# Performance work log

Hardware: AMD Instinct MI355X
Metric: run time of the kernel (lower is better)

## Reference

```python
import jax, jax.numpy as jnp
import numpy as np

WS, SS, NH = 7, 3, 16  # window_size, shift_size, num_heads


def _rel_pos_index(ws):
    coords = np.stack(np.meshgrid(np.arange(ws), np.arange(ws), indexing='ij'))  # (2, ws, ws)
    cf = coords.reshape(2, -1)                       # (2, N)
    rel = (cf[:, :, None] - cf[:, None, :]).transpose(1, 2, 0).copy()  # (N, N, 2)
    rel[:, :, 0] += ws - 1
    rel[:, :, 1] += ws - 1
    rel[:, :, 0] *= 2 * ws - 1
    return rel.sum(-1)                               # (N, N) int indices into bias table


def _attn_mask(Hp, Wp, ws, ss):
    img = np.zeros((Hp, Wp))
    slices = (slice(0, -ws), slice(-ws, -ss), slice(-ss, None))
    cnt = 0
    for h in slices:
        for w in slices:
            img[h, w] = cnt
            cnt += 1
    mw = img.reshape(Hp // ws, ws, Wp // ws, ws).transpose(0, 2, 1, 3).reshape(-1, ws * ws)  # (nW, N)
    am = mw[:, None, :] - mw[:, :, None]             # (nW, N, N)
    return np.where(am != 0, -100.0, 0.0).astype(np.float32)


def setup_inputs() -> dict:
    key = jax.random.key(0)
    k1, k2, k3, k4 = jax.random.split(key, 4)
    B, H, W, C = 16, 56, 56, 512
    return {
        'q_out': jax.random.normal(k1, (B, H, W, C), dtype=jnp.float32),
        'k_out': jax.random.normal(k2, (B, H, W, C), dtype=jnp.float32),
        'v_out': jax.random.normal(k3, (B, H, W, C), dtype=jnp.float32),
        'bias_table': 0.02 * jax.random.normal(k4, ((2 * WS - 1) ** 2, NH), dtype=jnp.float32),
        'C': C, 'H': H, 'W': W,
        'x_low_padding_h': 0, 'x_low_padding_w': 0,
    }


def reference(q_out, k_out, v_out, bias_table, C, H, W, x_low_padding_h, x_low_padding_w):
    ws, ss, nh = WS, SS, NH
    Hp, Wp = H + x_low_padding_h, W + x_low_padding_w
    B = q_out.shape[0]
    hd = C // nh
    scale = hd ** (-0.5)
    N = ws * ws

    def part(x):  # (B,Hp,Wp,C) -> (B*nW, N, C)
        x = x.reshape(B, Hp // ws, ws, Wp // ws, ws, C).transpose(0, 1, 3, 2, 4, 5)
        return x.reshape(-1, N, C)

    # cyclic shift
    sq = jnp.roll(q_out, (-ss, -ss), axis=(1, 2))
    sk = jnp.roll(k_out, (-ss, -ss), axis=(1, 2))
    sv = jnp.roll(v_out, (-ss, -ss), axis=(1, 2))

    qw, kw, vw = part(sq), part(sk), part(sv)
    B_ = qw.shape[0]
    q = qw.reshape(B_, N, nh, hd).transpose(0, 2, 1, 3) * scale  # (B_, nh, N, hd)
    k = kw.reshape(B_, N, nh, hd).transpose(0, 2, 1, 3)
    v = vw.reshape(B_, N, nh, hd).transpose(0, 2, 1, 3)

    attn = jnp.einsum('bhnd,bhmd->bhnm', q, k)  # (B_, nh, N, N)

    # relative position bias
    rpi = _rel_pos_index(ws)
    bias = bias_table[rpi.reshape(-1)].reshape(N, N, nh).transpose(2, 0, 1)  # (nh, N, N)
    attn = attn + bias[None]

    # shift mask
    am = jnp.asarray(_attn_mask(Hp, Wp, ws, ss), dtype=attn.dtype)  # (nW, N, N)
    nW = am.shape[0]
    attn = attn.reshape(B_ // nW, nW, nh, N, N) + am[None, :, None]
    attn = jax.nn.softmax(attn.reshape(B_, nh, N, N), axis=-1)

    xw = jnp.einsum('bhnm,bhmd->bhnd', attn, v).transpose(0, 2, 1, 3).reshape(B_, N, C)

    # window reverse + reverse shift
    x = xw.reshape(B, Hp // ws, Wp // ws, ws, ws, C).transpose(0, 1, 3, 2, 4, 5).reshape(B, Hp, Wp, C)
    return jnp.roll(x, (ss, ss), axis=(1, 2))
```

## Files before the change

### kernel.cpp

```cpp
#include <hip/hip_runtime.h>
#include <stdint.h>


constexpr int WSZ  = 7;
constexpr int NTOK = 49;
constexpr int NH_  = 16;
constexpr int HD_  = 32;
constexpr int SP   = 56;
constexpr int CH   = 512;
constexpr float LOG2E = 1.4426950408889634f;

typedef float    f32x4 __attribute__((ext_vector_type(4)));
typedef short    s16x8 __attribute__((ext_vector_type(8)));
typedef _Float16 f16x4 __attribute__((ext_vector_type(4)));

union FragU { uint32_t w[4]; s16x8 v; };

__device__ __forceinline__ uint32_t bf16_hibits(float x) {
    uint32_t u = __float_as_uint(x);
    u += 0x7fffu + ((u >> 16) & 1u);
    return u & 0xffff0000u;
}
__device__ __forceinline__ uint32_t pk_bf16(float a, float b) {
    return (bf16_hibits(a) >> 16) | bf16_hibits(b);
}

__global__ __launch_bounds__(256)
void build_bm(const float* __restrict__ bias, _Float16* __restrict__ bm)
{
    const int blk = blockIdx.x;
    const int h = blk >> 2, cls = blk & 3;
    for (int idx = threadIdx.x; idx < 4096; idx += 256) {
        const int q = idx >> 6, m = idx & 63;
        float val;
        if (q >= NTOK || m >= NTOK) {
            val = -1000.0f;
        } else {
            const int iq = q / 7, jq = q % 7, im = m / 7, jm = m % 7;
            const int rpi = (iq - im + 6) * 13 + (jq - jm + 6);
            const float bv = bias[rpi * NH_ + h];
            const int rq = ((cls & 2) ? (iq < 4 ? 3 : 6) : 0)
                         + ((cls & 1) ? (jq < 4 ? 1 : 2) : 0);
            const int rm = ((cls & 2) ? (im < 4 ? 3 : 6) : 0)
                         + ((cls & 1) ? (jm < 4 ? 1 : 2) : 0);
            const float mask = (rq != rm) ? -100.0f : 0.0f;
            val = (bv + mask) * LOG2E;
        }
        bm[blk * 4096 + idx] = (_Float16)val;
    }
}

struct Raw {
    float4 q[4][2];
    float4 k[4][2];
    float  v[2][2][8];
};
struct Frag {
    s16x8 Qh[4], Kh[4], Vb[2][2];
};

__device__ __forceinline__ int make_off(int wh, int lane) {
    const int h  = wh & 15;
    const int w  = wh >> 4;
    const int wc = w & 7, wr = (w >> 3) & 7, b = w >> 6;
    const int t  = lane < NTOK ? lane : NTOK - 1;
    const int it = t / 7, jt = t - 7 * it;
    int sr = wr * 7 + it + 3; if (sr >= SP) sr -= SP;
    int sc = wc * 7 + jt + 3; if (sc >= SP) sc -= SP;
    return ((b * SP + sr) * SP + sc) * CH + h * HD_;
}
__device__ __forceinline__ int cls_of(int wh) {
    const int w = wh >> 4;
    return ((((w >> 3) & 7) == 7) ? 2 : 0) | (((w & 7) == 7) ? 1 : 0);
}

__device__ __forceinline__ void issue_qkv(const float* __restrict__ qg,
                                          const float* __restrict__ kg,
                                          const float* __restrict__ vg,
                                          int off, int l16, int g, Raw& r) {
    int oQK[4];
#pragma unroll
    for (int tt = 0; tt < 4; ++tt) oQK[tt] = __shfl(off, 16 * tt + l16);
    int oV[16];
#pragma unroll
    for (int mc = 0; mc < 2; ++mc)
#pragma unroll
        for (int e = 0; e < 8; ++e) oV[8 * mc + e] = __shfl(off, 32 * mc + 8 * g + e);
#pragma unroll
    for (int tt = 0; tt < 4; ++tt) {
        const float* qp = qg + oQK[tt] + 8 * g;
        const float* kp = kg + oQK[tt] + 8 * g;
        r.q[tt][0] = *(const float4*)qp;  r.q[tt][1] = *(const float4*)(qp + 4);
        r.k[tt][0] = *(const float4*)kp;  r.k[tt][1] = *(const float4*)(kp + 4);
    }
#pragma unroll
    for (int mc = 0; mc < 2; ++mc)
#pragma unroll
        for (int dh = 0; dh < 2; ++dh)
#pragma unroll
            for (int e = 0; e < 8; ++e)
                r.v[mc][dh][e] = vg[oV[8 * mc + e] + 16 * dh + l16];
}

__device__ __forceinline__ void convertQKV(const Raw& r, float qs, Frag& f) {
#pragma unroll
    for (int tt = 0; tt < 4; ++tt) {
        FragU qh, kh;
        qh.w[0] = pk_bf16(r.q[tt][0].x * qs, r.q[tt][0].y * qs);
        qh.w[1] = pk_bf16(r.q[tt][0].z * qs, r.q[tt][0].w * qs);
        qh.w[2] = pk_bf16(r.q[tt][1].x * qs, r.q[tt][1].y * qs);
        qh.w[3] = pk_bf16(r.q[tt][1].z * qs, r.q[tt][1].w * qs);
        kh.w[0] = pk_bf16(r.k[tt][0].x, r.k[tt][0].y);
        kh.w[1] = pk_bf16(r.k[tt][0].z, r.k[tt][0].w);
        kh.w[2] = pk_bf16(r.k[tt][1].x, r.k[tt][1].y);
        kh.w[3] = pk_bf16(r.k[tt][1].z, r.k[tt][1].w);
        f.Qh[tt] = qh.v; f.Kh[tt] = kh.v;
    }
#pragma unroll
    for (int mc = 0; mc < 2; ++mc)
#pragma unroll
        for (int dh = 0; dh < 2; ++dh) {
            FragU fu;
#pragma unroll
            for (int wd = 0; wd < 4; ++wd)
                fu.w[wd] = pk_bf16(r.v[mc][dh][2 * wd], r.v[mc][dh][2 * wd + 1]);
            f.Vb[mc][dh] = fu.v;
        }
}

__device__ __forceinline__ void load_bm(const _Float16* __restrict__ bmh,
                                        int l16, int g, f16x4 (&bmr)[4][4]) {
#pragma unroll
    for (int tq = 0; tq < 4; ++tq)
#pragma unroll
        for (int tk = 0; tk < 4; ++tk)
            bmr[tq][tk] = *(const f16x4*)(bmh + (16 * tq + l16) * 64 + 16 * tk + 4 * g);
}

__device__ __forceinline__ void do_math(const Frag& f, const f16x4 (&bmr)[4][4],
                                        int off, int lane, int g, int l16,
                                        float* __restrict__ outg) {
    uint32_t u0[4][4], u1[4][4];
    float inv[4];
#pragma unroll
    for (int tq = 0; tq < 4; ++tq) {
        float dsum = 0.f;
#pragma unroll
        for (int tk = 0; tk < 4; ++tk) {
            f32x4 a;
            a[0] = (float)bmr[tq][tk][0] - 23.f;
            a[1] = (float)bmr[tq][tk][1] - 23.f;
            a[2] = (float)bmr[tq][tk][2] - 23.f;
            a[3] = (float)bmr[tq][tk][3] - 23.f;
            a = __builtin_amdgcn_mfma_f32_16x16x32_bf16(f.Kh[tk], f.Qh[tq], a, 0, 0, 0);
            float e0 = __builtin_amdgcn_exp2f(a[0]);
            float e1 = __builtin_amdgcn_exp2f(a[1]);
            float e2 = __builtin_amdgcn_exp2f(a[2]);
            float e3 = __builtin_amdgcn_exp2f(a[3]);
            dsum += (e0 + e1) + (e2 + e3);
            u0[tq][tk] = pk_bf16(e0, e1);
            u1[tq][tk] = pk_bf16(e2, e3);
        }
        dsum += __shfl_xor(dsum, 16);
        dsum += __shfl_xor(dsum, 32);
        inv[tq] = 1.0f / (dsum + 1e-30f);
    }

    const int srcb = 32 * (g & 1) + l16;
    const bool hiG = (lane >= 32);
    s16x8 PA[4][2];
#pragma unroll
    for (int tq = 0; tq < 4; ++tq)
#pragma unroll
        for (int mc = 0; mc < 2; ++mc) {
            FragU fu;
#pragma unroll
            for (int wd = 0; wd < 4; ++wd) {
                const int sl = srcb + 16 * (wd >> 1);
                uint32_t A, B;
                if (wd & 1) {
                    A = __shfl(u1[tq][2 * mc],     sl);
                    B = __shfl(u1[tq][2 * mc + 1], sl);
                } else {
                    A = __shfl(u0[tq][2 * mc],     sl);
                    B = __shfl(u0[tq][2 * mc + 1], sl);
                }
                fu.w[wd] = hiG ? B : A;
            }
            PA[tq][mc] = fu.v;
        }

#pragma unroll
    for (int tq = 0; tq < 4; ++tq) {
        f32x4 acc[2];
#pragma unroll
        for (int dh = 0; dh < 2; ++dh) {
            f32x4 a = {0.f, 0.f, 0.f, 0.f};
            a = __builtin_amdgcn_mfma_f32_16x16x32_bf16(PA[tq][0], f.Vb[0][dh], a, 0, 0, 0);
            a = __builtin_amdgcn_mfma_f32_16x16x32_bf16(PA[tq][1], f.Vb[1][dh], a, 0, 0, 0);
            acc[dh] = a;
        }
#pragma unroll
        for (int r = 0; r < 4; ++r) {
            const float iv = __shfl(inv[tq], 4 * g + r);
            const int oo = __shfl(off, 16 * tq + 4 * g + r);
            if (tq < 3 || (g == 0 && r == 0)) {
#pragma unroll
                for (int dh = 0; dh < 2; ++dh)
                    outg[oo + 16 * dh + l16] = acc[dh][r] * iv;
            }
        }
    }
}

__global__ __launch_bounds__(256, 2)
void swin_pipe_kernel(const float* __restrict__ qg,
                      const float* __restrict__ kg,
                      const float* __restrict__ vg,
                      const _Float16* __restrict__ bm,
                      float* __restrict__ outg)
{
    const int wave = threadIdx.x >> 6;
    const int gw   = blockIdx.x * 4 + wave;
    const int lane = threadIdx.x & 63;
    const int g    = lane >> 4;
    const int l16  = lane & 15;
    const float qs = 0.17677669529663687f * LOG2E;

    const int h = gw & 15;
    const _Float16* bmhead = bm + (size_t)h * 4 * 4096;

    Raw A, B;
    Frag f;
    f16x4 bmr[4][4];

    const int wh0 = gw;
    const int off0 = make_off(wh0, lane);
    issue_qkv(qg, kg, vg, off0, l16, g, A);

    convertQKV(A, qs, f);
    load_bm(bmhead + cls_of(wh0) * 4096, l16, g, bmr);
    const int wh1 = gw + 4096;
    const int off1 = make_off(wh1, lane);
    issue_qkv(qg, kg, vg, off1, l16, g, B);
    __builtin_amdgcn_sched_barrier(0);
    do_math(f, bmr, off0, lane, g, l16, outg);

    convertQKV(B, qs, f);
    load_bm(bmhead + cls_of(wh1) * 4096, l16, g, bmr);
    const int wh2 = gw + 8192;
    const int off2 = make_off(wh2, lane);
    issue_qkv(qg, kg, vg, off2, l16, g, A);
    __builtin_amdgcn_sched_barrier(0);
    do_math(f, bmr, off1, lane, g, l16, outg);

    convertQKV(A, qs, f);
    load_bm(bmhead + cls_of(wh2) * 4096, l16, g, bmr);
    const int wh3 = gw + 12288;
    const int off3 = make_off(wh3, lane);
    issue_qkv(qg, kg, vg, off3, l16, g, B);
    __builtin_amdgcn_sched_barrier(0);
    do_math(f, bmr, off2, lane, g, l16, outg);

    convertQKV(B, qs, f);
    load_bm(bmhead + cls_of(wh3) * 4096, l16, g, bmr);
    __builtin_amdgcn_sched_barrier(0);
    do_math(f, bmr, off3, lane, g, l16, outg);
}

__global__ __launch_bounds__(256)
void swin_block_scalar(const float* __restrict__ qg,
                       const float* __restrict__ kg,
                       const float* __restrict__ vg,
                       const float* __restrict__ bias,
                       float* __restrict__ outg)
{
    const int wave = __builtin_amdgcn_readfirstlane(threadIdx.x >> 6);
    const int wh   = blockIdx.x * 4 + wave;
    const int h    = wh & (NH_ - 1);
    const int w    = wh >> 4;
    const int wc   = w & 7;
    const int wr   = (w >> 3) & 7;
    const int b    = w >> 6;

    const int lane = threadIdx.x & 63;
    const int rr   = lane < NTOK ? lane : NTOK - 1;
    const int i    = rr / WSZ;
    const int j    = rr - i * WSZ;

    const int hp = wr * WSZ + i;
    const int wp = wc * WSZ + j;
    int sr = hp + 3; if (sr >= SP) sr -= SP;
    int sc = wp + 3; if (sc >= SP) sc -= SP;
    const int rowoff = ((b * SP + sr) * SP + sc) * CH + h * HD_;
    const int reg_r = (hp < 49 ? 0 : (hp < 53 ? 3 : 6))
                    + (wp < 49 ? 0 : (wp < 53 ? 1 : 2));
    const float qscale = 0.17677669529663687f * LOG2E;

    float qr[HD_];
    {
        const float4* qp = reinterpret_cast<const float4*>(qg + rowoff);
#pragma unroll
        for (int tt = 0; tt < HD_ / 4; ++tt) {
            float4 x = qp[tt];
            qr[4*tt+0] = x.x * qscale; qr[4*tt+1] = x.y * qscale;
            qr[4*tt+2] = x.z * qscale; qr[4*tt+3] = x.w * qscale;
        }
    }
    const int biaslane = (i * 13 + j) * 16 + h;
    float o[HD_];
#pragma unroll
    for (int d = 0; d < HD_; ++d) o[d] = 0.f;
    float denom = 0.f;
    const float* kb = kg + b * SP * SP * CH + h * HD_;
    const float* vb = vg + b * SP * SP * CH + h * HD_;

    for (int ic = 0; ic < WSZ; ++ic) {
        const int hpc = wr * WSZ + ic;
        int src_r = hpc + 3; if (src_r >= SP) src_r -= SP;
        const int regh_c = (hpc < 49 ? 0 : (hpc < 53 ? 3 : 6));
        const float* krow0 = kb + src_r * SP * CH;
        const float* vrow0 = vb + src_r * SP * CH;
        float e[WSZ];
#pragma unroll
        for (int u = 0; u < WSZ; ++u) {
            const int wpc = wc * WSZ + u;
            int src_c = wpc + 3; if (src_c >= SP) src_c -= SP;
            const int reg_c = regh_c + (wpc < 49 ? 0 : (wpc < 53 ? 1 : 2));
            const float* krow = krow0 + src_c * CH;
            const float bv = bias[biaslane + ((6 - ic) * 13 + (6 - u)) * 16];
            float s0 = fmaf(bv, LOG2E, (reg_r != reg_c) ? -167.26950408889634f : -23.0f);
            float s1 = 0.f, s2 = 0.f, s3 = 0.f;
#pragma unroll
            for (int d = 0; d < HD_; d += 4) {
                s0 = fmaf(qr[d+0], krow[d+0], s0);
                s1 = fmaf(qr[d+1], krow[d+1], s1);
                s2 = fmaf(qr[d+2], krow[d+2], s2);
                s3 = fmaf(qr[d+3], krow[d+3], s3);
            }
            e[u] = exp2f((s0 + s1) + (s2 + s3));
            denom += e[u];
        }
#pragma unroll
        for (int u = 0; u < WSZ; ++u) {
            const int wpc = wc * WSZ + u;
            int src_c = wpc + 3; if (src_c >= SP) src_c -= SP;
            const float* vrow = vrow0 + src_c * CH;
            const float ev = e[u];
#pragma unroll
            for (int d = 0; d < HD_; ++d) o[d] = fmaf(ev, vrow[d], o[d]);
        }
    }
    const float invd = 1.0f / denom;
    if (lane < NTOK) {
        float4* op = reinterpret_cast<float4*>(outg + rowoff);
#pragma unroll
        for (int tt = 0; tt < HD_ / 4; ++tt) {
            float4 x;
            x.x = o[4*tt+0] * invd; x.y = o[4*tt+1] * invd;
            x.z = o[4*tt+2] * invd; x.w = o[4*tt+3] * invd;
            op[tt] = x;
        }
    }
}

extern "C" void kernel_launch(void* const* d_in, const int* in_sizes, int n_in,
                              void* d_out, int out_size, void* d_ws, size_t ws_size,
                              hipStream_t stream) {
    const float* q    = (const float*)d_in[0];
    const float* k    = (const float*)d_in[1];
    const float* v    = (const float*)d_in[2];
    const float* bias = (const float*)d_in[3];
    float* out        = (float*)d_out;

    const int B   = in_sizes[0] / (SP * SP * CH);
    const int nwh = B * (SP / WSZ) * (SP / WSZ) * NH_;

    const size_t bm_bytes = (size_t)NH_ * 4 * 4096 * sizeof(_Float16);
    if (ws_size >= bm_bytes) {
        _Float16* bm = (_Float16*)d_ws;
        hipLaunchKernelGGL(build_bm, dim3(NH_ * 4), dim3(256), 0, stream, bias, bm);
        hipLaunchKernelGGL(swin_pipe_kernel, dim3(nwh / 16), dim3(256), 0, stream,
                           q, k, v, bm, out);
    } else {
        hipLaunchKernelGGL(swin_block_scalar, dim3(nwh / 4), dim3(256), 0, stream,
                           q, k, v, bias, out);
    }
}
```

Baseline: 111.6 us.

## Stage Q/K window loads through LDS with direct global-to-LDS loads

Q and K tiles for the next window are now loaded with global_load_lds into a per-wave 16KB LDS slot, instead of into double-buffered register structs. They are read back and converted to bf16 after an explicit vmcnt(0) wait. V stays on the register path, still double-buffered. The aim is to cut VGPR pressure from holding two raw fp32 Q/K/V sets, so more loads can be in flight or occupancy can rise. The cost is 64KB of dynamic LDS per block, an extra LDS round trip, and a full vmcnt drain that also waits on the previous window's output stores.

```diff
diff --git a/kernel.cpp b/kernel.cpp
--- a/kernel.cpp
+++ b/kernel.cpp
@@ -10,6 +10,9 @@
 constexpr int CH   = 512;
 constexpr float LOG2E = 1.4426950408889634f;
 
+constexpr int SLOT_BYTES = 16384;
+constexpr size_t LDS_BYTES = 4 * SLOT_BYTES;
+
 typedef float    f32x4 __attribute__((ext_vector_type(4)));
 typedef short    s16x8 __attribute__((ext_vector_type(8)));
 typedef _Float16 f16x4 __attribute__((ext_vector_type(4)));
@@ -23,6 +26,13 @@
 }
 __device__ __forceinline__ uint32_t pk_bf16(float a, float b) {
     return (bf16_hibits(a) >> 16) | bf16_hibits(b);
+}
+
+__device__ __forceinline__ void glds16(const float* g, void* l) {
+    __builtin_amdgcn_global_load_lds(
+        (const __attribute__((address_space(1))) uint32_t*)g,
+        (__attribute__((address_space(3))) uint32_t*)l,
+        16, 0, 0);
 }
 
 __global__ __launch_bounds__(256)
@@ -50,11 +60,6 @@
     }
 }
 
-struct Raw {
-    float4 q[4][2];
-    float4 k[4][2];
-    float  v[2][2][8];
-};
 struct Frag {
     s16x8 Qh[4], Kh[4], Vb[2][2];
 };
@@ -74,46 +79,57 @@
     return ((((w >> 3) & 7) == 7) ? 2 : 0) | (((w & 7) == 7) ? 1 : 0);
 }
 
-__device__ __forceinline__ void issue_qkv(const float* __restrict__ qg,
-                                          const float* __restrict__ kg,
-                                          const float* __restrict__ vg,
-                                          int off, int l16, int g, Raw& r) {
-    int oQK[4];
-#pragma unroll
-    for (int tt = 0; tt < 4; ++tt) oQK[tt] = __shfl(off, 16 * tt + l16);
+__device__ __forceinline__ void issue_glds(const float* __restrict__ qg,
+                                           const float* __restrict__ kg,
+                                           int off, int l16, int g, char* slot) {
+#pragma unroll
+    for (int tt = 0; tt < 4; ++tt) {
+        const int o = __shfl(off, 16 * tt + l16);
+        const float* qp = qg + o + 8 * g;
+        const float* kp = kg + o + 8 * g;
+        glds16(qp,     slot + (tt * 2 + 0) * 1024);
+        glds16(qp + 4, slot + (tt * 2 + 1) * 1024);
+        glds16(kp,     slot + 8192 + (tt * 2 + 0) * 1024);
+        glds16(kp + 4, slot + 8192 + (tt * 2 + 1) * 1024);
+    }
+}
+
+__device__ __forceinline__ void issue_v(const float* __restrict__ vg,
+                                        int off, int l16, int g,
+                                        float (&v)[2][2][8]) {
     int oV[16];
 #pragma unroll
     for (int mc = 0; mc < 2; ++mc)
 #pragma unroll
-        for (int e = 0; e < 8; ++e) oV[8 * mc + e] = __shfl(off, 32 * mc + 8 * g + e);
+        for (int e = 0; e < 8; ++e)
+            oV[8 * mc + e] = __shfl(off, 32 * mc + 8 * g + e);
+#pragma unroll
+    for (int mc = 0; mc < 2; ++mc)
+#pragma unroll
+        for (int dh = 0; dh < 2; ++dh)
+#pragma unroll
+            for (int e = 0; e < 8; ++e)
+                v[mc][dh][e] = vg[oV[8 * mc + e] + 16 * dh + l16];
+}
+
+__device__ __forceinline__ void readback_convert(const char* slot,
+                                                 const float (&v)[2][2][8],
+                                                 float qs, int lane, Frag& f) {
 #pragma unroll
     for (int tt = 0; tt < 4; ++tt) {
-        const float* qp = qg + oQK[tt] + 8 * g;
-        const float* kp = kg + oQK[tt] + 8 * g;
-        r.q[tt][0] = *(const float4*)qp;  r.q[tt][1] = *(const float4*)(qp + 4);
-        r.k[tt][0] = *(const float4*)kp;  r.k[tt][1] = *(const float4*)(kp + 4);
-    }
-#pragma unroll
-    for (int mc = 0; mc < 2; ++mc)
-#pragma unroll
-        for (int dh = 0; dh < 2; ++dh)
-#pragma unroll
-            for (int e = 0; e < 8; ++e)
-                r.v[mc][dh][e] = vg[oV[8 * mc + e] + 16 * dh + l16];
-}
-
-__device__ __forceinline__ void convertQKV(const Raw& r, float qs, Frag& f) {
-#pragma unroll
-    for (int tt = 0; tt < 4; ++tt) {
+        const float4 q0 = *(const float4*)(slot + (tt * 2 + 0) * 1024 + lane * 16);
+        const float4 q1 = *(const float4*)(slot + (tt * 2 + 1) * 1024 + lane * 16);
+        const float4 k0 = *(const float4*)(slot + 8192 + (tt * 2 + 0) * 1024 + lane * 16);
+        const float4 k1 = *(const float4*)(slot + 8192 + (tt * 2 + 1) * 1024 + lane * 16);
         FragU qh, kh;
-        qh.w[0] = pk_bf16(r.q[tt][0].x * qs, r.q[tt][0].y * qs);
-        qh.w[1] = pk_bf16(r.q[tt][0].z * qs, r.q[tt][0].w * qs);
-        qh.w[2] = pk_bf16(r.q[tt][1].x * qs, r.q[tt][1].y * qs);
-        qh.w[3] = pk_bf16(r.q[tt][1].z * qs, r.q[tt][1].w * qs);
-        kh.w[0] = pk_bf16(r.k[tt][0].x, r.k[tt][0].y);
-        kh.w[1] = pk_bf16(r.k[tt][0].z, r.k[tt][0].w);
-        kh.w[2] = pk_bf16(r.k[tt][1].x, r.k[tt][1].y);
-        kh.w[3] = pk_bf16(r.k[tt][1].z, r.k[tt][1].w);
+        qh.w[0] = pk_bf16(q0.x * qs, q0.y * qs);
+        qh.w[1] = pk_bf16(q0.z * qs, q0.w * qs);
+        qh.w[2] = pk_bf16(q1.x * qs, q1.y * qs);
+        qh.w[3] = pk_bf16(q1.z * qs, q1.w * qs);
+        kh.w[0] = pk_bf16(k0.x, k0.y);
+        kh.w[1] = pk_bf16(k0.z, k0.w);
+        kh.w[2] = pk_bf16(k1.x, k1.y);
+        kh.w[3] = pk_bf16(k1.z, k1.w);
         f.Qh[tt] = qh.v; f.Kh[tt] = kh.v;
     }
 #pragma unroll
@@ -123,7 +139,7 @@
             FragU fu;
 #pragma unroll
             for (int wd = 0; wd < 4; ++wd)
-                fu.w[wd] = pk_bf16(r.v[mc][dh][2 * wd], r.v[mc][dh][2 * wd + 1]);
+                fu.w[wd] = pk_bf16(v[mc][dh][2 * wd], v[mc][dh][2 * wd + 1]);
             f.Vb[mc][dh] = fu.v;
         }
 }
@@ -213,14 +229,21 @@
     }
 }
 
+__device__ __forceinline__ void wait_vmem() {
+    asm volatile("s_waitcnt vmcnt(0)" ::: "memory");
+    __builtin_amdgcn_sched_barrier(0);
+}
+
 __global__ __launch_bounds__(256, 2)
-void swin_pipe_kernel(const float* __restrict__ qg,
+void swin_glds_kernel(const float* __restrict__ qg,
                       const float* __restrict__ kg,
                       const float* __restrict__ vg,
                       const _Float16* __restrict__ bm,
                       float* __restrict__ outg)
 {
+    extern __shared__ char smem[];
     const int wave = threadIdx.x >> 6;
+    char* slot = smem + wave * SLOT_BYTES;
     const int gw   = blockIdx.x * 4 + wave;
     const int lane = threadIdx.x & 63;
     const int g    = lane >> 4;
@@ -230,39 +253,50 @@
     const int h = gw & 15;
     const _Float16* bmhead = bm + (size_t)h * 4 * 4096;
 
-    Raw A, B;
+    float VA[2][2][8], VB[2][2][8];
     Frag f;
     f16x4 bmr[4][4];
 
     const int wh0 = gw;
     const int off0 = make_off(wh0, lane);
-    issue_qkv(qg, kg, vg, off0, l16, g, A);
-
-    convertQKV(A, qs, f);
+    issue_glds(qg, kg, off0, l16, g, slot);
+    issue_v(vg, off0, l16, g, VA);
+
+    wait_vmem();
+    readback_convert(slot, VA, qs, lane, f);
     load_bm(bmhead + cls_of(wh0) * 4096, l16, g, bmr);
+    __builtin_amdgcn_sched_barrier(0);
     const int wh1 = gw + 4096;
     const int off1 = make_off(wh1, lane);
-    issue_qkv(qg, kg, vg, off1, l16, g, B);
+    issue_glds(qg, kg, off1, l16, g, slot);
+    issue_v(vg, off1, l16, g, VB);
     __builtin_amdgcn_sched_barrier(0);
     do_math(f, bmr, off0, lane, g, l16, outg);
 
-    convertQKV(B, qs, f);
+    wait_vmem();
+    readback_convert(slot, VB, qs, lane, f);
     load_bm(bmhead + cls_of(wh1) * 4096, l16, g, bmr);
+    __builtin_amdgcn_sched_barrier(0);
     const int wh2 = gw + 8192;
     const int off2 = make_off(wh2, lane);
-    issue_qkv(qg, kg, vg, off2, l16, g, A);
+    issue_glds(qg, kg, off2, l16, g, slot);
+    issue_v(vg, off2, l16, g, VA);
     __builtin_amdgcn_sched_barrier(0);
     do_math(f, bmr, off1, lane, g, l16, outg);
 
-    convertQKV(A, qs, f);
+    wait_vmem();
+    readback_convert(slot, VA, qs, lane, f);
     load_bm(bmhead + cls_of(wh2) * 4096, l16, g, bmr);
+    __builtin_amdgcn_sched_barrier(0);
     const int wh3 = gw + 12288;
     const int off3 = make_off(wh3, lane);
-    issue_qkv(qg, kg, vg, off3, l16, g, B);
+    issue_glds(qg, kg, off3, l16, g, slot);
+    issue_v(vg, off3, l16, g, VB);
     __builtin_amdgcn_sched_barrier(0);
     do_math(f, bmr, off2, lane, g, l16, outg);
 
-    convertQKV(B, qs, f);
+    wait_vmem();
+    readback_convert(slot, VB, qs, lane, f);
     load_bm(bmhead + cls_of(wh3) * 4096, l16, g, bmr);
     __builtin_amdgcn_sched_barrier(0);
     do_math(f, bmr, off3, lane, g, l16, outg);
@@ -379,9 +413,12 @@
     const size_t bm_bytes = (size_t)NH_ * 4 * 4096 * sizeof(_Float16);
     if (ws_size >= bm_bytes) {
         _Float16* bm = (_Float16*)d_ws;
+        (void)hipFuncSetAttribute(
+            reinterpret_cast<const void*>(swin_glds_kernel),
+            hipFuncAttributeMaxDynamicSharedMemorySize, (int)LDS_BYTES);
         hipLaunchKernelGGL(build_bm, dim3(NH_ * 4), dim3(256), 0, stream, bias, bm);
-        hipLaunchKernelGGL(swin_pipe_kernel, dim3(nwh / 16), dim3(256), 0, stream,
-                           q, k, v, bm, out);
+        hipLaunchKernelGGL(swin_glds_kernel, dim3(nwh / 16), dim3(256), LDS_BYTES,
+                           stream, q, k, v, bm, out);
     } else {
         hipLaunchKernelGGL(swin_block_scalar, dim3(nwh / 4), dim3(256), 0, stream,
                            q, k, v, bias, out);
```

Result: slower. 115.1 us (+3.2%).
